# Kernel optimization log

Hardware: AMD Instinct MI355X
Metric: run time of the kernel (lower is better)

The kernel has to match this reference:

```python
import jax, jax.numpy as jnp
import numpy as np

NUM_USR = 8192
H = 256  # NUM_SOURCE == H (feature dim of y_a); NUM_TARGET = 256


def setup_inputs() -> dict:
    key = jax.random.key(0)
    k1, k2, k3, k4 = jax.random.split(key, 4)
    return {
        "y_a": jax.random.normal(k1, (NUM_USR, H), dtype=jnp.float32),
        "y_b": jax.random.normal(k2, (NUM_USR, H), dtype=jnp.float32),
        "W": jax.random.normal(k3, (H, H), dtype=jnp.float32) * (1.0 / np.sqrt(H)),
        "b": jax.random.normal(k4, (H,), dtype=jnp.float32) * 0.01,
    }


def reference(y_a, y_b, W, b):
    # Linear: proj[j] = W @ y_b[j] + b   (torch nn.Linear convention)
    proj = jnp.einsum("jt,st->js", y_b, W) + b          # [num_usr, H]
    # torch loop computes score[i, j] = y_a[i] . proj[j], replicated H times
    # then averaged: out[i, k] = (1/H) * sum_j sigmoid(score[i, j])
    scores = jnp.einsum("ih,jh->ij", y_a, proj)          # [num_usr, num_usr]
    s = jnp.sum(jax.nn.sigmoid(scores), axis=1) / y_a.shape[1]  # [num_usr]
    return jnp.broadcast_to(s[:, None], y_a.shape)       # [num_usr, H]
```

## Files before the change

### kernel.cpp

```cpp
#include <hip/hip_runtime.h>

#define NUSR 8192
#define HDIM 256

typedef __attribute__((ext_vector_type(8))) __bf16 bf16x8;
typedef __attribute__((ext_vector_type(4))) float f32x4;

union frag_u { bf16x8 v; unsigned short u[8]; unsigned int d[4]; };

__device__ __forceinline__ unsigned int f2bf(float f) {
  unsigned u = __builtin_bit_cast(unsigned, f);
  u += 0x7FFFu + ((u >> 16) & 1u);
  return u >> 16;
}
__device__ __forceinline__ unsigned int f2bf2(float lo, float hi) {
  return f2bf(lo) | (f2bf(hi) << 16);
}
__device__ __forceinline__ float sigmoidf_fast(float x) {
  float e = __builtin_amdgcn_exp2f(x * -1.44269504088896340736f);
  return __builtin_amdgcn_rcpf(1.0f + e);
}


__global__ __launch_bounds__(256) void k1_fused(
    const float* __restrict__ ya, const float* __restrict__ yb,
    const float* __restrict__ W, const float* __restrict__ bvec,
    unsigned short* __restrict__ yabf, unsigned short* __restrict__ PX,
    float* __restrict__ svec)
{
  const int b   = blockIdx.x;
  const int tid = threadIdx.x;

  if (b < 256) {
    const int lane = tid & 63;
    const int w    = tid >> 6;
    const int q    = lane >> 4;
    const int i    = lane & 15;

    frag_u B[2][8];
#pragma unroll
    for (int g = 0; g < 2; ++g) {
      const float* ybrow = yb + (size_t)(b * 32 + g * 16 + i) * HDIM;
#pragma unroll
      for (int kb = 0; kb < 8; ++kb) {
        float4 v0 = *(const float4*)&ybrow[kb * 32 + q * 8];
        float4 v1 = *(const float4*)&ybrow[kb * 32 + q * 8 + 4];
        B[g][kb].d[0] = f2bf2(v0.x, v0.y); B[g][kb].d[1] = f2bf2(v0.z, v0.w);
        B[g][kb].d[2] = f2bf2(v1.x, v1.y); B[g][kb].d[3] = f2bf2(v1.z, v1.w);
      }
    }

#pragma unroll
    for (int t = 0; t < 4; ++t) {
      const int st = w * 4 + t;
      f32x4 acc[2] = {{0.f,0.f,0.f,0.f},{0.f,0.f,0.f,0.f}};
#pragma unroll
      for (int kb = 0; kb < 8; ++kb) {
        const float* wr = W + (size_t)(st * 16 + i) * HDIM + kb * 32 + q * 8;
        float4 w0 = *(const float4*)wr;
        float4 w1 = *(const float4*)(wr + 4);
        frag_u Af;
        Af.d[0] = f2bf2(w0.x, w0.y); Af.d[1] = f2bf2(w0.z, w0.w);
        Af.d[2] = f2bf2(w1.x, w1.y); Af.d[3] = f2bf2(w1.z, w1.w);
#pragma unroll
        for (int g = 0; g < 2; ++g)
          acc[g] = __builtin_amdgcn_mfma_f32_16x16x32_bf16(Af.v, B[g][kb].v, acc[g], 0, 0, 0);
      }
      float4 bias = *(const float4*)&bvec[st * 16 + q * 4];
#pragma unroll
      for (int g = 0; g < 2; ++g) {
        const int jg = b * 2 + g;
        unsigned v0 = f2bf2(acc[g][0] + bias.x, acc[g][1] + bias.y);
        unsigned v1 = f2bf2(acc[g][2] + bias.z, acc[g][3] + bias.w);
        size_t off = (size_t)jg * 4096 + (size_t)(st >> 1) * 512
                   + (size_t)(((st & 1) << 1) | (q >> 1)) * 128 + i * 8 + ((q & 1) * 4);
        *(uint2*)(PX + off) = make_uint2(v0, v1);
      }
    }
  } else {
    const int id = (b - 256) * 256 + tid;
    const float4* src = (const float4*)ya;
    uint4* dst = (uint4*)yabf;
#pragma unroll
    for (int u = 0; u < 4; ++u) {
      int d = id + u * 65536;
      float4 a = src[d * 2];
      float4 c = src[d * 2 + 1];
      uint4 o = { f2bf2(a.x, a.y), f2bf2(a.z, a.w),
                  f2bf2(c.x, c.y), f2bf2(c.z, c.w) };
      dst[d] = o;
    }
    if (b == 511) {
      float4 z = {0.f, 0.f, 0.f, 0.f};
      float4* sv = (float4*)svec;
#pragma unroll
      for (int u = 0; u < 8; ++u) sv[u * 256 + tid] = z;
    }
  }
}

__global__ __launch_bounds__(256, 2) void k2_score(
    const unsigned short* __restrict__ yabf, const unsigned short* __restrict__ PX,
    float* __restrict__ svec)
{
  const int tid  = threadIdx.x;
  const int lane = tid & 63;
  const int w    = tid >> 6;
  const int quad = lane >> 4;
  const int l15  = lane & 15;

  const int bid = blockIdx.x;
  const int xcd = bid & 7;
  const int k   = bid >> 3;
  const int by  = xcd * 2 + (k >> 5);
  const int bx  = k & 31;

  const int rbase = bx * 256 + w * 64;
  const int cg16  = by * 32;

  frag_u A[4][8];
#pragma unroll
  for (int g = 0; g < 4; ++g) {
    const unsigned short* src = yabf + (size_t)(rbase + g * 16 + l15) * HDIM;
#pragma unroll
    for (int kb = 0; kb < 8; ++kb)
      A[g][kb].v = *(const bf16x8*)&src[kb * 32 + quad * 8];
  }

  const unsigned short* psrc = PX + (size_t)cg16 * 4096;

  float rs[4][4] = {{0.f,0.f,0.f,0.f},{0.f,0.f,0.f,0.f},
                    {0.f,0.f,0.f,0.f},{0.f,0.f,0.f,0.f}};

  frag_u Ba[8], Bb[8];

#define LOADSEG(DST, SEG)                                                   \
  do {                                                                      \
    const unsigned short* _s = psrc + (size_t)(SEG) * 4096;                 \
    _Pragma("unroll")                                                       \
    for (int kb = 0; kb < 8; ++kb)                                          \
      DST[kb].v = *(const bf16x8*)&_s[kb * 512 + lane * 8];                 \
  } while (0)

#define COMPUTESEG(BUF)                                                     \
  do {                                                                      \
    f32x4 acc[4] = {{0.f,0.f,0.f,0.f},{0.f,0.f,0.f,0.f},                    \
                    {0.f,0.f,0.f,0.f},{0.f,0.f,0.f,0.f}};                   \
    _Pragma("unroll")                                                       \
    for (int kb = 0; kb < 8; ++kb) {                                        \
      _Pragma("unroll")                                                     \
      for (int g = 0; g < 4; ++g)                                           \
        acc[g] = __builtin_amdgcn_mfma_f32_16x16x32_bf16(                   \
            A[g][kb].v, BUF[kb].v, acc[g], 0, 0, 0);                        \
    }                                                                       \
    _Pragma("unroll")                                                       \
    for (int g = 0; g < 4; ++g)                                             \
      _Pragma("unroll")                                                     \
      for (int r = 0; r < 4; ++r)                                           \
        rs[g][r] += sigmoidf_fast(acc[g][r]);                               \
  } while (0)

  LOADSEG(Ba, 0);

  for (int t = 0; t < 16; ++t) {
    LOADSEG(Bb, 2 * t + 1);
    COMPUTESEG(Ba);
    if (t < 15)
      LOADSEG(Ba, 2 * t + 2);
    COMPUTESEG(Bb);
  }
#undef LOADSEG
#undef COMPUTESEG

#pragma unroll
  for (int off = 1; off < 16; off <<= 1)
#pragma unroll
    for (int g = 0; g < 4; ++g)
#pragma unroll
      for (int r = 0; r < 4; ++r)
        rs[g][r] += __shfl_xor(rs[g][r], off, 64);

  if (l15 == 0) {
#pragma unroll
    for (int g = 0; g < 4; ++g)
#pragma unroll
      for (int r = 0; r < 4; ++r)
        atomicAdd(&svec[rbase + g * 16 + quad * 4 + r], rs[g][r]);
  }
}

__global__ __launch_bounds__(256) void k3_bcast(
    const float* __restrict__ svec, float* __restrict__ out)
{
  int idx = blockIdx.x * 256 + threadIdx.x;
  int row = idx >> 6;
  float v = svec[row] * (1.0f / 256.0f);
  float4 o = {v, v, v, v};
  ((float4*)out)[idx] = o;
}

extern "C" void kernel_launch(void* const* d_in, const int* in_sizes, int n_in,
                              void* d_out, int out_size, void* d_ws, size_t ws_size,
                              hipStream_t stream) {
  (void)in_sizes; (void)n_in; (void)out_size;
  const float* ya = (const float*)d_in[0];
  const float* yb = (const float*)d_in[1];
  const float* W  = (const float*)d_in[2];
  const float* bv = (const float*)d_in[3];
  float* out = (float*)d_out;

  char* ws = (char*)d_ws;
  unsigned short *PX, *yabf;
  float* svec;
  const size_t need = (8ull << 20) + (32ull << 10);
  if (ws_size >= need) {
    PX   = (unsigned short*)ws;
    yabf = (unsigned short*)(ws + (4 << 20));
    svec = (float*)(ws + (8 << 20));
  } else {
    PX   = (unsigned short*)d_out;
    yabf = (unsigned short*)((char*)d_out + (4 << 20));
    svec = (float*)ws;
  }

  k1_fused<<<512, 256, 0, stream>>>(ya, yb, W, bv, yabf, PX, svec);
  k2_score<<<512, 256, 0, stream>>>(yabf, PX, svec);
  k3_bcast<<<2048, 256, 0, stream>>>(svec, out);
}
```

Before: 120.3 us.

## Stage PX tiles through LDS with triple-buffered direct global-to-LDS loads

In the score kernel, each of the four waves used to load its own copy of the shared projection tile straight into registers. Now the block cooperatively stages each tile into shared memory with global_load_lds, triple-buffered, synchronised by vmcnt waits and a barrier. Waves then read B fragments from LDS, with s_setprio raised around the MFMA loop. This cuts redundant global and L2 traffic by four and frees registers, at the cost of LDS use (48KB per block), per-iteration barriers, and possibly lower occupancy.

```diff
diff --git a/kernel.cpp b/kernel.cpp
--- a/kernel.cpp
+++ b/kernel.cpp
@@ -103,6 +103,7 @@
     const unsigned short* __restrict__ yabf, const unsigned short* __restrict__ PX,
     float* __restrict__ svec)
 {
+  __shared__ __align__(16) unsigned short bs[3][8192];
   const int tid  = threadIdx.x;
   const int lane = tid & 63;
   const int w    = tid >> 6;
@@ -132,45 +133,57 @@
   float rs[4][4] = {{0.f,0.f,0.f,0.f},{0.f,0.f,0.f,0.f},
                     {0.f,0.f,0.f,0.f},{0.f,0.f,0.f,0.f}};
 
-  frag_u Ba[8], Bb[8];
-
-#define LOADSEG(DST, SEG)                                                   \
-  do {                                                                      \
-    const unsigned short* _s = psrc + (size_t)(SEG) * 4096;                 \
-    _Pragma("unroll")                                                       \
-    for (int kb = 0; kb < 8; ++kb)                                          \
-      DST[kb].v = *(const bf16x8*)&_s[kb * 512 + lane * 8];                 \
+#define STAGE(B, T)                                                          \
+  do {                                                                       \
+    const unsigned short* _src = psrc + (size_t)(T) * 8192;                  \
+    unsigned short* _dst = &bs[(B)][0];                                      \
+    _Pragma("unroll")                                                        \
+    for (int p = 0; p < 4; ++p) {                                            \
+      int c = p * 256 + tid;                                                 \
+      __builtin_amdgcn_global_load_lds(                                      \
+          (const __attribute__((address_space(1))) unsigned int*)(const void*)(_src + c * 8), \
+          (__attribute__((address_space(3))) unsigned int*)(void*)(_dst + c * 8), \
+          16, 0, 0);                                                         \
+    }                                                                        \
   } while (0)
 
-#define COMPUTESEG(BUF)                                                     \
-  do {                                                                      \
-    f32x4 acc[4] = {{0.f,0.f,0.f,0.f},{0.f,0.f,0.f,0.f},                    \
-                    {0.f,0.f,0.f,0.f},{0.f,0.f,0.f,0.f}};                   \
-    _Pragma("unroll")                                                       \
-    for (int kb = 0; kb < 8; ++kb) {                                        \
-      _Pragma("unroll")                                                     \
-      for (int g = 0; g < 4; ++g)                                           \
-        acc[g] = __builtin_amdgcn_mfma_f32_16x16x32_bf16(                   \
-            A[g][kb].v, BUF[kb].v, acc[g], 0, 0, 0);                        \
-    }                                                                       \
-    _Pragma("unroll")                                                       \
-    for (int g = 0; g < 4; ++g)                                             \
-      _Pragma("unroll")                                                     \
-      for (int r = 0; r < 4; ++r)                                           \
-        rs[g][r] += sigmoidf_fast(acc[g][r]);                               \
-  } while (0)
-
-  LOADSEG(Ba, 0);
-
+  STAGE(0, 0);
+  STAGE(1, 1);
+
+  int cb = 0, sb = 2;
   for (int t = 0; t < 16; ++t) {
-    LOADSEG(Bb, 2 * t + 1);
-    COMPUTESEG(Ba);
     if (t < 15)
-      LOADSEG(Ba, 2 * t + 2);
-    COMPUTESEG(Bb);
-  }
-#undef LOADSEG
-#undef COMPUTESEG
+      asm volatile("s_waitcnt vmcnt(4)" ::: "memory");
+    else
+      asm volatile("s_waitcnt vmcnt(0)" ::: "memory");
+    asm volatile("s_barrier" ::: "memory");
+    if (t < 14)
+      STAGE(sb, t + 2);
+
+    const unsigned short* buf = &bs[cb][0];
+#pragma unroll
+    for (int tt = 0; tt < 2; ++tt) {
+      f32x4 acc[4] = {{0.f,0.f,0.f,0.f},{0.f,0.f,0.f,0.f},
+                      {0.f,0.f,0.f,0.f},{0.f,0.f,0.f,0.f}};
+      __builtin_amdgcn_s_setprio(1);
+#pragma unroll
+      for (int kb = 0; kb < 8; ++kb) {
+        bf16x8 bfrag = *(const bf16x8*)&buf[(tt * 512 + kb * 64 + lane) * 8];
+#pragma unroll
+        for (int g = 0; g < 4; ++g)
+          acc[g] = __builtin_amdgcn_mfma_f32_16x16x32_bf16(A[g][kb].v, bfrag, acc[g], 0, 0, 0);
+      }
+      __builtin_amdgcn_s_setprio(0);
+#pragma unroll
+      for (int g = 0; g < 4; ++g)
+#pragma unroll
+        for (int r = 0; r < 4; ++r)
+          rs[g][r] += sigmoidf_fast(acc[g][r]);
+    }
+    cb = (cb == 2) ? 0 : cb + 1;
+    sb = (sb == 2) ? 0 : sb + 1;
+  }
+#undef STAGE
 
 #pragma unroll
   for (int off = 1; off < 16; off <<= 1)
```

After: 122.6 us. About the same (+1.9%).
